# Kernel tuning notes

Measured on AMD Instinct MI355X. Metric: run time of the kernel, lower is better.

The kernel has to match this reference:

```python
import jax, jax.numpy as jnp
from jax import lax
import numpy as np

WSTD = 0.1
BSTD = 0.1
DN = ("NHWC", "HWIO", "NHWC")  # matches tf.nn.convolution defaults


def setup_inputs() -> dict:
    key = jax.random.key(0)
    k1, k2, k3, k4, k5 = jax.random.split(key, 5)
    B, H, Wd, Cin, F, KH, KW = 32, 64, 64, 128, 256, 3, 3
    X = jax.random.normal(k1, (B, H, Wd, Cin), dtype=jnp.float32)
    # glorot-ish kernel
    fan = KH * KW * Cin
    W = jax.random.normal(k2, (KH, KW, Cin, F), dtype=jnp.float32) / np.float32(np.sqrt(fan))
    bias = 0.01 * jax.random.normal(k3, (F,), dtype=jnp.float32)
    # per-sample multiplicative errors: abs(1 + N(0, std)) as in A-Connect
    Werr = jnp.abs(1.0 + WSTD * jax.random.normal(k4, (B, KH, KW, Cin, F), dtype=jnp.float32))
    Berr = jnp.abs(1.0 + BSTD * jax.random.normal(k5, (B, F), dtype=jnp.float32))
    return {"X": X, "W": W, "bias": bias, "Werr": Werr, "Berr": Berr}


def reference(X, W, bias, Werr, Berr):
    # memW[b] = W * Werr[b]  -> per-sample perturbed kernels [B,KH,KW,Cin,F]
    memW = W[None] * Werr

    def conv1(x, k):  # x: [H,W,Cin], k: [KH,KW,Cin,F]
        return lax.conv_general_dilated(x[None], k, window_strides=(1, 1),
                                        padding="SAME", dimension_numbers=DN)[0]

    Z = jax.vmap(conv1)(X, memW)                 # [B,H,W,F]
    membias = bias[None] * Berr                  # [B,F]
    Z = Z + membias[:, None, None, :]
    return jax.nn.relu(Z)
```

## Files before the change

### kernel.cpp

```cpp
#include <hip/hip_runtime.h>

#define B_   32
#define H_   64
#define W_   64
#define CIN  128
#define F_   256
#define K_   1152
#define M_   4096

#define HP_   66
#define XPROW (66*128)
#define XPIMG (66*66*128)
#define XP_ELEMS ((size_t)B_ * XPIMG)
#define XP_BYTES (XP_ELEMS * 2)

#define WBT_BYTES ((size_t)B_ * F_ * K_ * 2)
#define FULL_WS   (WBT_BYTES + XP_BYTES + 256)
#define ZPAGE_OFF WBT_BYTES

#define BM_ 256
#define BK_ 64

typedef __attribute__((ext_vector_type(8))) short bf16x8;
typedef __attribute__((ext_vector_type(4))) float f32x4;

__device__ __forceinline__ unsigned pkbf(float a, float b) {
    unsigned ua = __builtin_bit_cast(unsigned, a) + 0x8000u;
    unsigned ub = __builtin_bit_cast(unsigned, b) + 0x8000u;
    return __builtin_amdgcn_perm(ub, ua, 0x07060302u);
}

__device__ __forceinline__ void async16(const void* g, void* l) {
    __builtin_amdgcn_global_load_lds(
        (const __attribute__((address_space(1))) unsigned int*)g,
        (__attribute__((address_space(3))) unsigned int*)l, 16, 0, 0);
}

__global__ void prep_kernel(const float* __restrict__ W,
                            const float* __restrict__ Werr,
                            const float* __restrict__ X,
                            unsigned short* __restrict__ WbT,
                            unsigned short* __restrict__ Xp,
                            unsigned int* __restrict__ zpage) {
    __shared__ float tile[32 * 68];
    int bid = blockIdx.x;
    int t   = threadIdx.x;

    if (bid < 4608) {
        int ft   = bid & 3;
        int rest = bid >> 2;
        int kt   = rest % 36;
        int b    = rest / 36;
        int k0 = kt * 32;
        int f0 = ft * 64;

        if (bid == 0 && t < 64) zpage[t] = 0u;

        #pragma unroll
        for (int i = 0; i < 2; ++i) {
            int c   = i * 256 + t;
            int kl  = c >> 4;
            int fl4 = c & 15;
            size_t src = (size_t)(k0 + kl) * F_ + f0 + fl4 * 4;
            f32x4 w4 = *(const f32x4*)&W[src];
            f32x4 e4 = *(const f32x4*)&Werr[(size_t)b * (K_ * F_) + src];
            f32x4 v  = w4 * e4;
            *(f32x4*)&tile[kl * 68 + fl4 * 4] = v;
        }
        __syncthreads();
        {
            int c  = t;
            int fl = c >> 2;
            int ku = c & 3;
            unsigned pk[4];
            #pragma unroll
            for (int j2 = 0; j2 < 4; ++j2) {
                float x0 = tile[(ku * 8 + j2 * 2 + 0) * 68 + fl];
                float x1 = tile[(ku * 8 + j2 * 2 + 1) * 68 + fl];
                pk[j2] = pkbf(x0, x1);
            }
            size_t dst = ((size_t)(b * F_ + f0 + fl)) * K_ + k0 + ku * 8;
            *(uint4*)&WbT[dst] = make_uint4(pk[0], pk[1], pk[2], pk[3]);
        }
    } else {
        int e = (bid - 4608) * 256 + t;
        int c16  = e & 15;
        int pos  = e >> 4;
        int wp   = pos % 66;
        int rest = pos / 66;
        int hp   = rest % 66;
        int b    = rest / 66;
        uint4 out;
        if (hp >= 1 && hp <= 64 && wp >= 1 && wp <= 64) {
            const float* src = X + (((size_t)b * 64 + (hp - 1)) * 64 + (wp - 1)) * 128
                                 + c16 * 8;
            f32x4 a = *(const f32x4*)src;
            f32x4 c = *(const f32x4*)(src + 4);
            out.x = pkbf(a[0], a[1]);  out.y = pkbf(a[2], a[3]);
            out.z = pkbf(c[0], c[1]);  out.w = pkbf(c[2], c[3]);
        } else {
            out = make_uint4(0u, 0u, 0u, 0u);
        }
        *(uint4*)&Xp[(size_t)e * 8] = out;
    }
}

__global__ void wbt_kernel(const float* __restrict__ W,
                           const float* __restrict__ Werr,
                           unsigned short* __restrict__ WbT,
                           unsigned int* __restrict__ zpage) {
    __shared__ float tile[32 * 68];
    int bid = blockIdx.x;
    int ft   = bid & 3;
    int rest = bid >> 2;
    int kt   = rest % 36;
    int b    = rest / 36;
    int k0 = kt * 32;
    int f0 = ft * 64;
    int t  = threadIdx.x;

    if (bid == 0 && t < 64) zpage[t] = 0u;

    #pragma unroll
    for (int i = 0; i < 2; ++i) {
        int c   = i * 256 + t;
        int kl  = c >> 4;
        int fl4 = c & 15;
        size_t src = (size_t)(k0 + kl) * F_ + f0 + fl4 * 4;
        f32x4 w4 = *(const f32x4*)&W[src];
        f32x4 e4 = *(const f32x4*)&Werr[(size_t)b * (K_ * F_) + src];
        f32x4 v  = w4 * e4;
        *(f32x4*)&tile[kl * 68 + fl4 * 4] = v;
    }
    __syncthreads();
    {
        int c  = t;
        int fl = c >> 2;
        int ku = c & 3;
        unsigned pk[4];
        #pragma unroll
        for (int j2 = 0; j2 < 4; ++j2) {
            float x0 = tile[(ku * 8 + j2 * 2 + 0) * 68 + fl];
            float x1 = tile[(ku * 8 + j2 * 2 + 1) * 68 + fl];
            pk[j2] = pkbf(x0, x1);
        }
        size_t dst = ((size_t)(b * F_ + f0 + fl)) * K_ + k0 + ku * 8;
        *(uint4*)&WbT[dst] = make_uint4(pk[0], pk[1], pk[2], pk[3]);
    }
}

__global__ __launch_bounds__(512, 2)
void gemm256_kernel(const unsigned short* __restrict__ Xp,
                    const unsigned short* __restrict__ WbT,
                    const float* __restrict__ bias,
                    const float* __restrict__ Berr,
                    float* __restrict__ Out) {
    __shared__ unsigned short As[2][BM_ * BK_];
    __shared__ unsigned short Bs[2][BM_ * BK_];

    int bid = blockIdx.x;
    int g   = (bid & 7) * 64 + (bid >> 3);
    int b   = g >> 4;
    int mt  = g & 15;
    int pm0 = mt * 256;

    int t    = threadIdx.x;
    int lane = t & 63;
    int wv   = t >> 6;
    int wm   = wv >> 2;
    int wn   = wv & 3;
    int l16  = lane & 15;
    int quad = lane >> 4;
    int swz  = (l16 & 7) << 4;

    const unsigned short* XpB = Xp + (size_t)b * XPIMG;
    const unsigned short* WbB = WbT + (size_t)b * F_ * K_;

    int aofs[4], bofs[4], ldst[4];
    #pragma unroll
    for (int p = 0; p < 4; ++p) {
        int c   = p * 512 + t;
        int row = c >> 3;
        int col = c & 7;
        int sc  = col ^ (row & 7);
        int m   = pm0 + row;
        int hb  = m >> 6, ww = m & 63;
        aofs[p] = hb * XPROW + ww * 128 + sc * 8;
        bofs[p] = row * K_ + sc * 8;
        ldst[p] = c * 8;
    }

    f32x4 acc[8][4];
    #pragma unroll
    for (int mi = 0; mi < 8; ++mi)
        #pragma unroll
        for (int ni = 0; ni < 4; ++ni)
            acc[mi][ni] = (f32x4){0.f, 0.f, 0.f, 0.f};

    #pragma unroll
    for (int p = 0; p < 4; ++p)
        async16(XpB + aofs[p], &As[0][ldst[p]]);
    #pragma unroll
    for (int p = 0; p < 4; ++p)
        async16(WbB + bofs[p], &Bs[0][ldst[p]]);
    asm volatile("s_waitcnt vmcnt(0)" ::: "memory");
    __builtin_amdgcn_s_barrier();

    for (int kt = 0; kt < 18; ++kt) {
        const int cur = kt & 1;
        const unsigned short* Acur = As[cur];
        const unsigned short* Bcur = Bs[cur];
        unsigned short* Anxt = As[cur ^ 1];
        unsigned short* Bnxt = Bs[cur ^ 1];
        const bool pf = (kt < 17);

        int ktn  = kt + 1;
        int khwN = ktn >> 1;
        int khN  = (khwN * 11) >> 5;
        int kwN  = khwN - khN * 3;
        int koA  = khN * XPROW + kwN * 128 + (ktn & 1) * 64;
        int koB  = ktn * 64;

        bf16x8 bfr[4];
        #pragma unroll
        for (int ks = 0; ks < 2; ++ks) {
            #pragma unroll
            for (int qm = 0; qm < 2; ++qm) {
                if (qm == 0) {
                    #pragma unroll
                    for (int ni = 0; ni < 4; ++ni) {
                        int row = wn * 64 + ni * 16 + l16;
                        bfr[ni] = *(const bf16x8*)((const char*)Bcur +
                                   ((row * 128 + quad * 16 + ks * 64) ^ swz));
                    }
                }
                bf16x8 af[4];
                #pragma unroll
                for (int mi = 0; mi < 4; ++mi) {
                    int row = wm * 128 + (qm * 4 + mi) * 16 + l16;
                    af[mi] = *(const bf16x8*)((const char*)Acur +
                              ((row * 128 + quad * 16 + ks * 64) ^ swz));
                }

                if (pf && ks == 0) {
                    if (qm == 0) {
                        #pragma unroll
                        for (int p = 0; p < 4; ++p)
                            async16(XpB + aofs[p] + koA, &Anxt[ldst[p]]);
                    } else {
                        #pragma unroll
                        for (int p = 0; p < 4; ++p)
                            async16(WbB + bofs[p] + koB, &Bnxt[ldst[p]]);
                    }
                }

                __builtin_amdgcn_s_barrier();

                __builtin_amdgcn_s_setprio(1);
                #pragma unroll
                for (int mi = 0; mi < 4; ++mi)
                    #pragma unroll
                    for (int ni = 0; ni < 4; ++ni)
                        acc[qm * 4 + mi][ni] = __builtin_amdgcn_mfma_f32_16x16x32_bf16(
                            af[mi], bfr[ni], acc[qm * 4 + mi][ni], 0, 0, 0);
                __builtin_amdgcn_s_setprio(0);

                if (ks == 1 && qm == 1) {
                    if (pf) asm volatile("s_waitcnt vmcnt(0)" ::: "memory");
                    __builtin_amdgcn_s_barrier();
                } else {
                    __builtin_amdgcn_s_barrier();
                }
            }
        }
    }

    float mb[4];
    #pragma unroll
    for (int ni = 0; ni < 4; ++ni) {
        int f = wn * 64 + ni * 16 + l16;
        mb[ni] = bias[f] * Berr[b * F_ + f];
    }
    #pragma unroll
    for (int mi = 0; mi < 8; ++mi) {
        #pragma unroll
        for (int rr = 0; rr < 4; ++rr) {
            int mm = pm0 + wm * 128 + mi * 16 + quad * 4 + rr;
            float* orow = Out + ((size_t)b * M_ + mm) * F_ + wn * 64;
            #pragma unroll
            for (int ni = 0; ni < 4; ++ni) {
                float v = acc[mi][ni][rr] + mb[ni];
                orow[ni * 16 + l16] = fmaxf(v, 0.0f);
            }
        }
    }
}

__global__ __launch_bounds__(256, 2)
void gemm_kernel_f32(const float* __restrict__ X,
                     const unsigned short* __restrict__ WbT,
                     const float* __restrict__ zpage,
                     const float* __restrict__ bias,
                     const float* __restrict__ Berr,
                     float* __restrict__ Out) {
    __shared__ unsigned short As[128 * 32];
    __shared__ unsigned short Bs[128 * 32];

    int bid = blockIdx.x;
    int g   = (bid & 7) | ((bid >> 8) << 3);
    int mt  = (bid >> 3) & 31;
    int b   = g >> 1;
    int nt  = g & 1;
    int pm0 = mt * 128;

    int t    = threadIdx.x;
    int lane = t & 63;
    int wv   = t >> 6;
    int wm   = wv >> 1;
    int wn   = wv & 1;
    int l16  = lane & 15;
    int quad = lane >> 4;

    int ml   = t >> 1;
    int half = t & 1;
    int m    = pm0 + ml;
    int hb   = m >> 6;
    int wwv  = m & 63;
    const float* Abase = X + (((size_t)b * 64 + hb - 1) * 64 + (wwv - 1)) * 128
                           + half * 16;
    unsigned vm = 0;
    #pragma unroll
    for (int khw = 0; khw < 9; ++khw) {
        int kh = (khw * 11) >> 5;
        int kw = khw - kh * 3;
        bool ok = ((unsigned)(hb + kh - 1) < 64u) && ((unsigned)(wwv + kw - 1) < 64u);
        vm |= (unsigned)ok << khw;
    }
    int ldsA = ml * 32 + half * 16;

    const unsigned short* wb = WbT + ((size_t)(b * F_ + nt * 128)) * K_;
    const unsigned short* Bbase[2];
    int ldsB[2];
    #pragma unroll
    for (int cc = 0; cc < 2; ++cc) {
        int c   = t + cc * 256;
        int nl  = c >> 2;
        int off = c & 3;
        Bbase[cc] = wb + (size_t)nl * K_ + off * 8;
        ldsB[cc]  = c * 8;
    }

    f32x4 acc[4][4];
    #pragma unroll
    for (int mi = 0; mi < 4; ++mi)
        #pragma unroll
        for (int ni = 0; ni < 4; ++ni)
            acc[mi][ni] = (f32x4){0.f, 0.f, 0.f, 0.f};

    f32x4 pr0, pr1, pr2, pr3;
    {
        const float* p = (vm & 1) ? Abase : zpage;
        pr0 = *(const f32x4*)(p);
        pr1 = *(const f32x4*)(p + 4);
        pr2 = *(const f32x4*)(p + 8);
        pr3 = *(const f32x4*)(p + 12);
    }

    for (int kt = 0; kt < 36; ++kt) {
        uint4 lo, hi;
        lo.x = pkbf(pr0[0], pr0[1]);  lo.y = pkbf(pr0[2], pr0[3]);
        lo.z = pkbf(pr1[0], pr1[1]);  lo.w = pkbf(pr1[2], pr1[3]);
        hi.x = pkbf(pr2[0], pr2[1]);  hi.y = pkbf(pr2[2], pr2[3]);
        hi.z = pkbf(pr3[0], pr3[1]);  hi.w = pkbf(pr3[2], pr3[3]);

        if (kt) __syncthreads();
        *(uint4*)&As[ldsA]     = lo;
        *(uint4*)&As[ldsA + 8] = hi;
        #pragma unroll
        for (int cc = 0; cc < 2; ++cc)
            async16(Bbase[cc] + kt * 32, &Bs[ldsB[cc]]);
        __syncthreads();

        if (kt < 35) {
            int ktn  = kt + 1;
            int khw  = ktn >> 2;
            int kh   = (khw * 11) >> 5;
            int kw   = khw - kh * 3;
            int koff = kh * 8192 + kw * 128 + ((ktn & 3) << 5);
            const float* p = ((vm >> khw) & 1) ? Abase + koff : zpage;
            pr0 = *(const f32x4*)(p);
            pr1 = *(const f32x4*)(p + 4);
            pr2 = *(const f32x4*)(p + 8);
            pr3 = *(const f32x4*)(p + 12);
        }

        bf16x8 af[4], bf[4];
        #pragma unroll
        for (int i = 0; i < 4; ++i) {
            af[i] = *(const bf16x8*)&As[(wm * 64 + i * 16 + l16) * 32 + quad * 8];
            bf[i] = *(const bf16x8*)&Bs[(wn * 64 + i * 16 + l16) * 32 + quad * 8];
        }
        #pragma unroll
        for (int mi = 0; mi < 4; ++mi)
            #pragma unroll
            for (int ni = 0; ni < 4; ++ni)
                acc[mi][ni] = __builtin_amdgcn_mfma_f32_16x16x32_bf16(
                    af[mi], bf[ni], acc[mi][ni], 0, 0, 0);
    }

    float mb[4];
    #pragma unroll
    for (int ni = 0; ni < 4; ++ni) {
        int f = nt * 128 + wn * 64 + ni * 16 + l16;
        mb[ni] = bias[f] * Berr[b * F_ + f];
    }
    #pragma unroll
    for (int mi = 0; mi < 4; ++mi) {
        #pragma unroll
        for (int rr = 0; rr < 4; ++rr) {
            int mm = pm0 + wm * 64 + mi * 16 + quad * 4 + rr;
            float* orow = Out + ((size_t)b * M_ + mm) * F_ + nt * 128 + wn * 64;
            #pragma unroll
            for (int ni = 0; ni < 4; ++ni) {
                float v = acc[mi][ni][rr] + mb[ni];
                orow[ni * 16 + l16] = fmaxf(v, 0.0f);
            }
        }
    }
}

__global__ __launch_bounds__(256)
void fallback_kernel(const float* __restrict__ X, const float* __restrict__ W,
                     const float* __restrict__ bias, const float* __restrict__ Werr,
                     const float* __restrict__ Berr, float* __restrict__ Out) {
    __shared__ float Xs[3 * 66 * 128];
    int bid = blockIdx.x;
    int b = bid >> 6;
    int h = bid & 63;
    int t = threadIdx.x;
    int f = t;

    for (int e = t; e < 3 * 66 * 128; e += 256) {
        int kh  = e / (66 * 128);
        int rem = e - kh * 66 * 128;
        int w66 = rem >> 7;
        int c   = rem & 127;
        int hh = h + kh - 1, ww = w66 - 1;
        float v = 0.f;
        if (hh >= 0 && hh < 64 && ww >= 0 && ww < 64)
            v = X[(((size_t)b * 64 + hh) * 64 + ww) * 128 + c];
        Xs[e] = v;
    }
    __syncthreads();

    float acc[64];
    #pragma unroll
    for (int w = 0; w < 64; ++w) acc[w] = 0.f;

    for (int kk = 0; kk < 9; ++kk) {
        int kh = (kk * 11) >> 5;
        int kw = kk - kh * 3;
        for (int c = 0; c < 128; ++c) {
            size_t wi = ((size_t)kk * 128 + c) * 256 + f;
            float wvv = W[wi] * Werr[(size_t)b * (K_ * F_) + wi];
            const float* xr = &Xs[(kh * 66 + kw) * 128 + c];
            #pragma unroll
            for (int w = 0; w < 64; ++w)
                acc[w] = fmaf(xr[w * 128], wvv, acc[w]);
        }
    }
    float mb = bias[f] * Berr[b * 256 + f];
    for (int w = 0; w < 64; ++w)
        Out[(((size_t)b * 64 + h) * 64 + w) * 256 + f] = fmaxf(acc[w] + mb, 0.f);
}

extern "C" void kernel_launch(void* const* d_in, const int* in_sizes, int n_in,
                              void* d_out, int out_size, void* d_ws, size_t ws_size,
                              hipStream_t stream) {
    const float* X    = (const float*)d_in[0];
    const float* W    = (const float*)d_in[1];
    const float* bias = (const float*)d_in[2];
    const float* Werr = (const float*)d_in[3];
    const float* Berr = (const float*)d_in[4];
    float* Out = (float*)d_out;

    if (ws_size >= FULL_WS) {
        unsigned short* WbT = (unsigned short*)d_ws;
        unsigned short* Xp  = (unsigned short*)((char*)d_ws + WBT_BYTES);
        unsigned int*   zpg = (unsigned int*)((char*)d_ws + WBT_BYTES + XP_BYTES);
        prep_kernel<<<4608 + 8712, 256, 0, stream>>>(W, Werr, X, WbT, Xp, zpg);
        gemm256_kernel<<<512, 512, 0, stream>>>(Xp, WbT, bias, Berr, Out);
    } else if (ws_size >= WBT_BYTES + 256) {
        unsigned short* WbT  = (unsigned short*)d_ws;
        unsigned int*   zpg  = (unsigned int*)((char*)d_ws + ZPAGE_OFF);
        wbt_kernel<<<B_ * 36 * 4, 256, 0, stream>>>(W, Werr, WbT, zpg);
        gemm_kernel_f32<<<B_ * 32 * 2, 256, 0, stream>>>(X, WbT, (const float*)zpg,
                                                         bias, Berr, Out);
    } else {
        fallback_kernel<<<B_ * 64, 256, 0, stream>>>(X, W, bias, Werr, Berr, Out);
    }
}
```

Before: 311.2 us.

## Spread prefetch loads across phases and use partial vmcnt waits

Each k-tile's global-to-LDS prefetch is split into four two-load groups, one per compute phase. B is issued first and A last, so the wait before the next tile only needs `vmcnt(2)` rather than a full drain. Address math is simplified to one base offset plus per-row-unit strides, which frees the per-thread offset arrays and their registers. The risk is LDS ordering: the partial waits must be correct for the A rows read early in the next iteration, and the changed load order could add memory stalls.

After: 297.0 us. -4.6%, faster.

```diff
diff --git a/kernel.cpp b/kernel.cpp
--- a/kernel.cpp
+++ b/kernel.cpp
@@ -176,19 +176,12 @@
     const unsigned short* XpB = Xp + (size_t)b * XPIMG;
     const unsigned short* WbB = WbT + (size_t)b * F_ * K_;
 
-    int aofs[4], bofs[4], ldst[4];
-    #pragma unroll
-    for (int p = 0; p < 4; ++p) {
-        int c   = p * 512 + t;
-        int row = c >> 3;
-        int col = c & 7;
-        int sc  = col ^ (row & 7);
-        int m   = pm0 + row;
-        int hb  = m >> 6, ww = m & 63;
-        aofs[p] = hb * XPROW + ww * 128 + sc * 8;
-        bofs[p] = row * K_ + sc * 8;
-        ldst[p] = c * 8;
-    }
+    int tr   = t >> 3;
+    int sc   = (t & 7) ^ (tr & 7);
+    int aoff = tr * 128 + sc * 8;
+    int boff = tr * K_ + sc * 8;
+    int mbase = mt * 4;
+    int ldof = t * 8;
 
     f32x4 acc[8][4];
     #pragma unroll
@@ -197,21 +190,25 @@
         for (int ni = 0; ni < 4; ++ni)
             acc[mi][ni] = (f32x4){0.f, 0.f, 0.f, 0.f};
 
-    #pragma unroll
-    for (int p = 0; p < 4; ++p)
-        async16(XpB + aofs[p], &As[0][ldst[p]]);
-    #pragma unroll
-    for (int p = 0; p < 4; ++p)
-        async16(WbB + bofs[p], &Bs[0][ldst[p]]);
-    asm volatile("s_waitcnt vmcnt(0)" ::: "memory");
+    auto stageA = [&](int bs, int ru, int ko) {
+        async16(XpB + (size_t)(mbase + ru) * XPROW + aoff + ko,
+                &As[bs][ru * 4096 + ldof]);
+    };
+    auto stageB = [&](int bs, int ru, int ko) {
+        async16(WbB + (size_t)ru * (64 * K_) + boff + ko,
+                &Bs[bs][ru * 4096 + ldof]);
+    };
+
+    stageB(0, 0, 0); stageB(0, 1, 0); stageB(0, 2, 0); stageB(0, 3, 0);
+    stageA(0, 0, 0); stageA(0, 2, 0); stageA(0, 1, 0); stageA(0, 3, 0);
+    asm volatile("s_waitcnt vmcnt(2)" ::: "memory");
     __builtin_amdgcn_s_barrier();
 
     for (int kt = 0; kt < 18; ++kt) {
         const int cur = kt & 1;
-        const unsigned short* Acur = As[cur];
-        const unsigned short* Bcur = Bs[cur];
-        unsigned short* Anxt = As[cur ^ 1];
-        unsigned short* Bnxt = Bs[cur ^ 1];
+        const int nxt = cur ^ 1;
+        const unsigned short* Ac = As[cur];
+        const unsigned short* Bc = Bs[cur];
         const bool pf = (kt < 17);
 
         int ktn  = kt + 1;
@@ -221,58 +218,88 @@
         int koA  = khN * XPROW + kwN * 128 + (ktn & 1) * 64;
         int koB  = ktn * 64;
 
-        bf16x8 bfr[4];
-        #pragma unroll
-        for (int ks = 0; ks < 2; ++ks) {
-            #pragma unroll
-            for (int qm = 0; qm < 2; ++qm) {
-                if (qm == 0) {
-                    #pragma unroll
-                    for (int ni = 0; ni < 4; ++ni) {
-                        int row = wn * 64 + ni * 16 + l16;
-                        bfr[ni] = *(const bf16x8*)((const char*)Bcur +
-                                   ((row * 128 + quad * 16 + ks * 64) ^ swz));
-                    }
-                }
-                bf16x8 af[4];
-                #pragma unroll
-                for (int mi = 0; mi < 4; ++mi) {
-                    int row = wm * 128 + (qm * 4 + mi) * 16 + l16;
-                    af[mi] = *(const bf16x8*)((const char*)Acur +
-                              ((row * 128 + quad * 16 + ks * 64) ^ swz));
-                }
-
-                if (pf && ks == 0) {
-                    if (qm == 0) {
-                        #pragma unroll
-                        for (int p = 0; p < 4; ++p)
-                            async16(XpB + aofs[p] + koA, &Anxt[ldst[p]]);
-                    } else {
-                        #pragma unroll
-                        for (int p = 0; p < 4; ++p)
-                            async16(WbB + bofs[p] + koB, &Bnxt[ldst[p]]);
-                    }
-                }
-
-                __builtin_amdgcn_s_barrier();
-
-                __builtin_amdgcn_s_setprio(1);
-                #pragma unroll
-                for (int mi = 0; mi < 4; ++mi)
-                    #pragma unroll
-                    for (int ni = 0; ni < 4; ++ni)
-                        acc[qm * 4 + mi][ni] = __builtin_amdgcn_mfma_f32_16x16x32_bf16(
-                            af[mi], bfr[ni], acc[qm * 4 + mi][ni], 0, 0, 0);
-                __builtin_amdgcn_s_setprio(0);
-
-                if (ks == 1 && qm == 1) {
-                    if (pf) asm volatile("s_waitcnt vmcnt(0)" ::: "memory");
-                    __builtin_amdgcn_s_barrier();
-                } else {
-                    __builtin_amdgcn_s_barrier();
-                }
-            }
-        }
+        bf16x8 af[4], bfr[4];
+
+        #pragma unroll
+        for (int ni = 0; ni < 4; ++ni) {
+            int row = wn * 64 + ni * 16 + l16;
+            bfr[ni] = *(const bf16x8*)((const char*)Bc + ((row * 128 + quad * 16) ^ swz));
+        }
+        #pragma unroll
+        for (int mi = 0; mi < 4; ++mi) {
+            int row = wm * 128 + mi * 16 + l16;
+            af[mi] = *(const bf16x8*)((const char*)Ac + ((row * 128 + quad * 16) ^ swz));
+        }
+        if (pf) { stageB(nxt, 0, koB); stageB(nxt, 1, koB); }
+        __builtin_amdgcn_s_barrier();
+        __builtin_amdgcn_s_setprio(1);
+        #pragma unroll
+        for (int mi = 0; mi < 4; ++mi)
+            #pragma unroll
+            for (int ni = 0; ni < 4; ++ni)
+                acc[mi][ni] = __builtin_amdgcn_mfma_f32_16x16x32_bf16(
+                    af[mi], bfr[ni], acc[mi][ni], 0, 0, 0);
+        __builtin_amdgcn_s_setprio(0);
+        if (pf) asm volatile("s_waitcnt vmcnt(2)" ::: "memory");
+        else    asm volatile("s_waitcnt vmcnt(0)" ::: "memory");
+        __builtin_amdgcn_s_barrier();
+
+        #pragma unroll
+        for (int mi = 0; mi < 4; ++mi) {
+            int row = wm * 128 + 64 + mi * 16 + l16;
+            af[mi] = *(const bf16x8*)((const char*)Ac + ((row * 128 + quad * 16) ^ swz));
+        }
+        if (pf) { stageB(nxt, 2, koB); stageB(nxt, 3, koB); }
+        __builtin_amdgcn_s_barrier();
+        __builtin_amdgcn_s_setprio(1);
+        #pragma unroll
+        for (int mi = 0; mi < 4; ++mi)
+            #pragma unroll
+            for (int ni = 0; ni < 4; ++ni)
+                acc[4 + mi][ni] = __builtin_amdgcn_mfma_f32_16x16x32_bf16(
+                    af[mi], bfr[ni], acc[4 + mi][ni], 0, 0, 0);
+        __builtin_amdgcn_s_setprio(0);
+        __builtin_amdgcn_s_barrier();
+
+        #pragma unroll
+        for (int ni = 0; ni < 4; ++ni) {
+            int row = wn * 64 + ni * 16 + l16;
+            bfr[ni] = *(const bf16x8*)((const char*)Bc + ((row * 128 + quad * 16 + 64) ^ swz));
+        }
+        #pragma unroll
+        for (int mi = 0; mi < 4; ++mi) {
+            int row = wm * 128 + mi * 16 + l16;
+            af[mi] = *(const bf16x8*)((const char*)Ac + ((row * 128 + quad * 16 + 64) ^ swz));
+        }
+        if (pf) { stageA(nxt, 0, koA); stageA(nxt, 2, koA); }
+        __builtin_amdgcn_s_barrier();
+        __builtin_amdgcn_s_setprio(1);
+        #pragma unroll
+        for (int mi = 0; mi < 4; ++mi)
+            #pragma unroll
+            for (int ni = 0; ni < 4; ++ni)
+                acc[mi][ni] = __builtin_amdgcn_mfma_f32_16x16x32_bf16(
+                    af[mi], bfr[ni], acc[mi][ni], 0, 0, 0);
+        __builtin_amdgcn_s_setprio(0);
+        __builtin_amdgcn_s_barrier();
+
+        #pragma unroll
+        for (int mi = 0; mi < 4; ++mi) {
+            int row = wm * 128 + 64 + mi * 16 + l16;
+            af[mi] = *(const bf16x8*)((const char*)Ac + ((row * 128 + quad * 16 + 64) ^ swz));
+        }
+        if (pf) { stageA(nxt, 1, koA); stageA(nxt, 3, koA); }
+        __builtin_amdgcn_s_barrier();
+        __builtin_amdgcn_s_setprio(1);
+        #pragma unroll
+        for (int mi = 0; mi < 4; ++mi)
+            #pragma unroll
+            for (int ni = 0; ni < 4; ++ni)
+                acc[4 + mi][ni] = __builtin_amdgcn_mfma_f32_16x16x32_bf16(
+                    af[mi], bfr[ni], acc[4 + mi][ni], 0, 0, 0);
+        __builtin_amdgcn_s_setprio(0);
+        if (pf) asm volatile("s_waitcnt vmcnt(2)" ::: "memory");
+        __builtin_amdgcn_s_barrier();
     }
 
     float mb[4];
```

## Restructure GEMM main loop into fine-grained half-tile async load pipeline

Applied to the files above, without the earlier changes.

Replaces the double-buffered K loop with a manually unrolled two-tile-per-iteration schedule. Global-to-LDS loads for the next tile are issued in half-tile chunks interleaved between MFMA phases, with partial vmcnt waits and scheduler barriers. The aim is to keep more loads in flight and overlap memory latency with compute more evenly. The cost is more barriers and a complex wait-count scheme that could easily be wrong or over-serialize.

After: 301.1 us. -3.2%, faster.

```diff
diff --git a/kernel.cpp b/kernel.cpp
--- a/kernel.cpp
+++ b/kernel.cpp
@@ -35,6 +35,9 @@
         (const __attribute__((address_space(1))) unsigned int*)g,
         (__attribute__((address_space(3))) unsigned int*)l, 16, 0, 0);
 }
+
+#define PHB do { __builtin_amdgcn_s_barrier(); \
+                 __builtin_amdgcn_sched_barrier(0); } while (0)
 
 __global__ void prep_kernel(const float* __restrict__ W,
                             const float* __restrict__ Werr,
@@ -176,18 +179,19 @@
     const unsigned short* XpB = Xp + (size_t)b * XPIMG;
     const unsigned short* WbB = WbT + (size_t)b * F_ * K_;
 
-    int aofs[4], bofs[4], ldst[4];
-    #pragma unroll
-    for (int p = 0; p < 4; ++p) {
-        int c   = p * 512 + t;
-        int row = c >> 3;
+    int asrc[2][2], bsrc[2][2];
+    #pragma unroll
+    for (int cc = 0; cc < 2; ++cc) {
+        int c   = t + cc * 512;
+        int r16 = c >> 3;
         int col = c & 7;
-        int sc  = col ^ (row & 7);
-        int m   = pm0 + row;
-        int hb  = m >> 6, ww = m & 63;
-        aofs[p] = hb * XPROW + ww * 128 + sc * 8;
-        bofs[p] = row * K_ + sc * 8;
-        ldst[p] = c * 8;
+        #pragma unroll
+        for (int h = 0; h < 2; ++h) {
+            int row = h * 128 + r16;
+            int sc  = col ^ (row & 7);
+            asrc[h][cc] = (mt * 4 + (row >> 6)) * XPROW + (row & 63) * 128 + sc * 8;
+            bsrc[h][cc] = row * K_ + sc * 8;
+        }
     }
 
     f32x4 acc[8][4];
@@ -197,82 +201,109 @@
         for (int ni = 0; ni < 4; ++ni)
             acc[mi][ni] = (f32x4){0.f, 0.f, 0.f, 0.f};
 
-    #pragma unroll
-    for (int p = 0; p < 4; ++p)
-        async16(XpB + aofs[p], &As[0][ldst[p]]);
-    #pragma unroll
-    for (int p = 0; p < 4; ++p)
-        async16(WbB + bofs[p], &Bs[0][ldst[p]]);
-    asm volatile("s_waitcnt vmcnt(0)" ::: "memory");
-    __builtin_amdgcn_s_barrier();
-
-    for (int kt = 0; kt < 18; ++kt) {
-        const int cur = kt & 1;
-        const unsigned short* Acur = As[cur];
-        const unsigned short* Bcur = Bs[cur];
-        unsigned short* Anxt = As[cur ^ 1];
-        unsigned short* Bnxt = Bs[cur ^ 1];
-        const bool pf = (kt < 17);
-
-        int ktn  = kt + 1;
-        int khwN = ktn >> 1;
-        int khN  = (khwN * 11) >> 5;
-        int kwN  = khwN - khN * 3;
-        int koA  = khN * XPROW + kwN * 128 + (ktn & 1) * 64;
-        int koB  = ktn * 64;
-
-        bf16x8 bfr[4];
-        #pragma unroll
-        for (int ks = 0; ks < 2; ++ks) {
+    auto stA = [&](int buf, int h, int ko) {
+        async16(XpB + asrc[h][0] + ko, &As[buf][h * 8192 + t * 8]);
+        async16(XpB + asrc[h][1] + ko, &As[buf][h * 8192 + 4096 + t * 8]);
+    };
+    auto stB = [&](int buf, int h, int ko) {
+        async16(WbB + bsrc[h][0] + ko, &Bs[buf][h * 8192 + t * 8]);
+        async16(WbB + bsrc[h][1] + ko, &Bs[buf][h * 8192 + 4096 + t * 8]);
+    };
+    auto rdB = [&](bf16x8* dst, const unsigned short* Bc, int ks) {
+        #pragma unroll
+        for (int ni = 0; ni < 4; ++ni) {
+            int row = wn * 64 + ni * 16 + l16;
+            dst[ni] = *(const bf16x8*)((const char*)Bc +
+                       ((row * 128 + quad * 16 + ks * 64) ^ swz));
+        }
+    };
+    auto rdA = [&](bf16x8* dst, const unsigned short* Ac, int qm, int ks) {
+        #pragma unroll
+        for (int mi = 0; mi < 4; ++mi) {
+            int row = wm * 128 + qm * 64 + mi * 16 + l16;
+            dst[mi] = *(const bf16x8*)((const char*)Ac +
+                       ((row * 128 + quad * 16 + ks * 64) ^ swz));
+        }
+    };
+    auto mm = [&](int qm, const bf16x8* a, const bf16x8* bb) {
+        __builtin_amdgcn_s_setprio(1);
+        #pragma unroll
+        for (int mi = 0; mi < 4; ++mi)
             #pragma unroll
-            for (int qm = 0; qm < 2; ++qm) {
-                if (qm == 0) {
-                    #pragma unroll
-                    for (int ni = 0; ni < 4; ++ni) {
-                        int row = wn * 64 + ni * 16 + l16;
-                        bfr[ni] = *(const bf16x8*)((const char*)Bcur +
-                                   ((row * 128 + quad * 16 + ks * 64) ^ swz));
-                    }
-                }
-                bf16x8 af[4];
-                #pragma unroll
-                for (int mi = 0; mi < 4; ++mi) {
-                    int row = wm * 128 + (qm * 4 + mi) * 16 + l16;
-                    af[mi] = *(const bf16x8*)((const char*)Acur +
-                              ((row * 128 + quad * 16 + ks * 64) ^ swz));
-                }
-
-                if (pf && ks == 0) {
-                    if (qm == 0) {
-                        #pragma unroll
-                        for (int p = 0; p < 4; ++p)
-                            async16(XpB + aofs[p] + koA, &Anxt[ldst[p]]);
-                    } else {
-                        #pragma unroll
-                        for (int p = 0; p < 4; ++p)
-                            async16(WbB + bofs[p] + koB, &Bnxt[ldst[p]]);
-                    }
-                }
-
-                __builtin_amdgcn_s_barrier();
-
-                __builtin_amdgcn_s_setprio(1);
-                #pragma unroll
-                for (int mi = 0; mi < 4; ++mi)
-                    #pragma unroll
-                    for (int ni = 0; ni < 4; ++ni)
-                        acc[qm * 4 + mi][ni] = __builtin_amdgcn_mfma_f32_16x16x32_bf16(
-                            af[mi], bfr[ni], acc[qm * 4 + mi][ni], 0, 0, 0);
-                __builtin_amdgcn_s_setprio(0);
-
-                if (ks == 1 && qm == 1) {
-                    if (pf) asm volatile("s_waitcnt vmcnt(0)" ::: "memory");
-                    __builtin_amdgcn_s_barrier();
-                } else {
-                    __builtin_amdgcn_s_barrier();
-                }
-            }
-        }
+            for (int ni = 0; ni < 4; ++ni)
+                acc[qm * 4 + mi][ni] = __builtin_amdgcn_mfma_f32_16x16x32_bf16(
+                    a[mi], bb[ni], acc[qm * 4 + mi][ni], 0, 0, 0);
+        __builtin_amdgcn_s_setprio(0);
+    };
+
+    stB(0, 0, 0); stB(0, 1, 0); stA(0, 0, 0); stA(0, 1, 0); stB(1, 0, 64);
+    asm volatile("s_waitcnt vmcnt(4)" ::: "memory");
+    PHB;
+
+    for (int p = 0; p < 9; ++p) {
+        const bool pf = (p < 8);
+        int kh_o = (p * 11) >> 5;
+        int kw_o = p - 3 * kh_o;
+        int koA_o = kh_o * XPROW + kw_o * 128 + 64;
+        int koB_o = (2 * p + 1) * 64;
+        int q1 = p + 1;
+        int kh_e = (q1 * 11) >> 5;
+        int kw_e = q1 - 3 * kh_e;
+        int koA_e2 = kh_e * XPROW + kw_e * 128;
+        int koB_e2 = (2 * p + 2) * 64;
+        int koB_o2 = (2 * p + 3) * 64;
+
+        const unsigned short* A0 = As[0]; const unsigned short* B0 = Bs[0];
+        const unsigned short* A1 = As[1]; const unsigned short* B1 = Bs[1];
+
+        bf16x8 bb[4], aa[4];
+
+        rdB(bb, B0, 0); rdA(aa, A0, 0, 0);
+        stB(1, 1, koB_o);
+        PHB;
+        mm(0, aa, bb);
+        asm volatile("s_waitcnt vmcnt(4)" ::: "memory");
+        PHB;
+        rdA(aa, A0, 1, 0);
+        stA(1, 0, koA_o);
+        PHB;
+        mm(1, aa, bb);
+        PHB;
+        rdB(bb, B0, 1); rdA(aa, A0, 0, 1);
+        stA(1, 1, koA_o);
+        PHB;
+        mm(0, aa, bb);
+        PHB;
+        rdA(aa, A0, 1, 1);
+        if (pf) stB(0, 0, koB_e2);
+        PHB;
+        mm(1, aa, bb);
+        if (pf) asm volatile("s_waitcnt vmcnt(4)" ::: "memory");
+        else    asm volatile("s_waitcnt vmcnt(2)" ::: "memory");
+        PHB;
+        rdB(bb, B1, 0); rdA(aa, A1, 0, 0);
+        if (pf) stB(0, 1, koB_e2);
+        PHB;
+        mm(0, aa, bb);
+        if (pf) asm volatile("s_waitcnt vmcnt(4)" ::: "memory");
+        else    asm volatile("s_waitcnt vmcnt(0)" ::: "memory");
+        PHB;
+        rdA(aa, A1, 1, 0);
+        if (pf) stA(0, 0, koA_e2);
+        PHB;
+        mm(1, aa, bb);
+        PHB;
+        rdB(bb, B1, 1); rdA(aa, A1, 0, 1);
+        if (pf) stA(0, 1, koA_e2);
+        PHB;
+        mm(0, aa, bb);
+        PHB;
+        rdA(aa, A1, 1, 1);
+        if (pf) stB(1, 0, koB_o2);
+        PHB;
+        mm(1, aa, bb);
+        if (pf) asm volatile("s_waitcnt vmcnt(4)" ::: "memory");
+        PHB;
     }
 
     float mb[4];
@@ -285,8 +316,8 @@
     for (int mi = 0; mi < 8; ++mi) {
         #pragma unroll
         for (int rr = 0; rr < 4; ++rr) {
-            int mm = pm0 + wm * 128 + mi * 16 + quad * 4 + rr;
-            float* orow = Out + ((size_t)b * M_ + mm) * F_ + wn * 64;
+            int mm2 = pm0 + wm * 128 + mi * 16 + quad * 4 + rr;
+            float* orow = Out + ((size_t)b * M_ + mm2) * F_ + wn * 64;
             #pragma unroll
             for (int ni = 0; ni < 4; ++ni) {
                 float v = acc[mi][ni][rr] + mb[ni];
```

## Switch conv GEMM to 128x256 tiles with triple-buffered BK=32 async pipeline

Applied to the files above, without the earlier changes.

The main bf16 GEMM moves from a 256x256 tile with BK=64 and double buffering to a 128x256 tile with BK=32 and a three-stage LDS ring. The launch doubles to 1024 blocks and the launch bound rises to 4 waves per SIMD. Prefetches now stay two stages ahead using partial vmcnt waits, with sched_barrier to stop the compiler reordering across phases. The goal is more occupancy and better latency hiding, at the cost of more B-tile reloads per output and less register reuse per block.

Measured after the change: 297.1 us. 1.05x faster.

```diff
diff --git a/kernel.cpp b/kernel.cpp
--- a/kernel.cpp
+++ b/kernel.cpp
@@ -18,9 +18,6 @@
 #define FULL_WS   (WBT_BYTES + XP_BYTES + 256)
 #define ZPAGE_OFF WBT_BYTES
 
-#define BM_ 256
-#define BK_ 64
-
 typedef __attribute__((ext_vector_type(8))) short bf16x8;
 typedef __attribute__((ext_vector_type(4))) float f32x4;
 
@@ -35,6 +32,9 @@
         (const __attribute__((address_space(1))) unsigned int*)g,
         (__attribute__((address_space(3))) unsigned int*)l, 16, 0, 0);
 }
+
+#define PHB do { __builtin_amdgcn_s_barrier(); \
+                 __builtin_amdgcn_sched_barrier(0); } while (0)
 
 __global__ void prep_kernel(const float* __restrict__ W,
                             const float* __restrict__ Werr,
@@ -149,20 +149,20 @@
     }
 }
 
-__global__ __launch_bounds__(512, 2)
-void gemm256_kernel(const unsigned short* __restrict__ Xp,
+__global__ __launch_bounds__(512, 4)
+void gemm128_kernel(const unsigned short* __restrict__ Xp,
                     const unsigned short* __restrict__ WbT,
                     const float* __restrict__ bias,
                     const float* __restrict__ Berr,
                     float* __restrict__ Out) {
-    __shared__ unsigned short As[2][BM_ * BK_];
-    __shared__ unsigned short Bs[2][BM_ * BK_];
+    __shared__ unsigned short As[3][128 * 32];
+    __shared__ unsigned short Bs[3][256 * 32];
 
     int bid = blockIdx.x;
-    int g   = (bid & 7) * 64 + (bid >> 3);
-    int b   = g >> 4;
-    int mt  = g & 15;
-    int pm0 = mt * 256;
+    int g   = (bid & 7) * 128 + (bid >> 3);
+    int b   = g >> 5;
+    int mt  = g & 31;
+    int pm0 = mt * 128;
 
     int t    = threadIdx.x;
     int lane = t & 63;
@@ -171,109 +171,82 @@
     int wn   = wv & 3;
     int l16  = lane & 15;
     int quad = lane >> 4;
-    int swz  = (l16 & 7) << 4;
+    int rswz = ((l16 >> 1) & 3) << 4;
 
     const unsigned short* XpB = Xp + (size_t)b * XPIMG;
     const unsigned short* WbB = WbT + (size_t)b * F_ * K_;
 
-    int aofs[4], bofs[4], ldst[4];
-    #pragma unroll
-    for (int p = 0; p < 4; ++p) {
-        int c   = p * 512 + t;
-        int row = c >> 3;
-        int col = c & 7;
-        int sc  = col ^ (row & 7);
-        int m   = pm0 + row;
-        int hb  = m >> 6, ww = m & 63;
-        aofs[p] = hb * XPROW + ww * 128 + sc * 8;
-        bofs[p] = row * K_ + sc * 8;
-        ldst[p] = c * 8;
-    }
-
-    f32x4 acc[8][4];
-    #pragma unroll
-    for (int mi = 0; mi < 8; ++mi)
+    int sc    = (t & 3) ^ ((t >> 3) & 3);
+    int arow  = t >> 2;
+    int aoff  = (mt * 2 + (arow >> 6)) * XPROW + (arow & 63) * 128 + sc * 8;
+    int boff0 = (t >> 2) * K_ + sc * 8;
+    int boff1 = (128 + (t >> 2)) * K_ + sc * 8;
+
+    f32x4 acc[4][4];
+    #pragma unroll
+    for (int mi = 0; mi < 4; ++mi)
         #pragma unroll
         for (int ni = 0; ni < 4; ++ni)
             acc[mi][ni] = (f32x4){0.f, 0.f, 0.f, 0.f};
 
-    #pragma unroll
-    for (int p = 0; p < 4; ++p)
-        async16(XpB + aofs[p], &As[0][ldst[p]]);
-    #pragma unroll
-    for (int p = 0; p < 4; ++p)
-        async16(WbB + bofs[p], &Bs[0][ldst[p]]);
-    asm volatile("s_waitcnt vmcnt(0)" ::: "memory");
-    __builtin_amdgcn_s_barrier();
-
-    for (int kt = 0; kt < 18; ++kt) {
-        const int cur = kt & 1;
-        const unsigned short* Acur = As[cur];
-        const unsigned short* Bcur = Bs[cur];
-        unsigned short* Anxt = As[cur ^ 1];
-        unsigned short* Bnxt = Bs[cur ^ 1];
-        const bool pf = (kt < 17);
-
-        int ktn  = kt + 1;
-        int khwN = ktn >> 1;
-        int khN  = (khwN * 11) >> 5;
-        int kwN  = khwN - khN * 3;
-        int koA  = khN * XPROW + kwN * 128 + (ktn & 1) * 64;
-        int koB  = ktn * 64;
-
-        bf16x8 bfr[4];
-        #pragma unroll
-        for (int ks = 0; ks < 2; ++ks) {
-            #pragma unroll
-            for (int qm = 0; qm < 2; ++qm) {
-                if (qm == 0) {
-                    #pragma unroll
-                    for (int ni = 0; ni < 4; ++ni) {
-                        int row = wn * 64 + ni * 16 + l16;
-                        bfr[ni] = *(const bf16x8*)((const char*)Bcur +
-                                   ((row * 128 + quad * 16 + ks * 64) ^ swz));
-                    }
-                }
-                bf16x8 af[4];
-                #pragma unroll
-                for (int mi = 0; mi < 4; ++mi) {
-                    int row = wm * 128 + (qm * 4 + mi) * 16 + l16;
-                    af[mi] = *(const bf16x8*)((const char*)Acur +
-                              ((row * 128 + quad * 16 + ks * 64) ^ swz));
-                }
-
-                if (pf && ks == 0) {
-                    if (qm == 0) {
-                        #pragma unroll
-                        for (int p = 0; p < 4; ++p)
-                            async16(XpB + aofs[p] + koA, &Anxt[ldst[p]]);
-                    } else {
-                        #pragma unroll
-                        for (int p = 0; p < 4; ++p)
-                            async16(WbB + bofs[p] + koB, &Bnxt[ldst[p]]);
-                    }
-                }
-
-                __builtin_amdgcn_s_barrier();
-
-                __builtin_amdgcn_s_setprio(1);
-                #pragma unroll
-                for (int mi = 0; mi < 4; ++mi)
-                    #pragma unroll
-                    for (int ni = 0; ni < 4; ++ni)
-                        acc[qm * 4 + mi][ni] = __builtin_amdgcn_mfma_f32_16x16x32_bf16(
-                            af[mi], bfr[ni], acc[qm * 4 + mi][ni], 0, 0, 0);
-                __builtin_amdgcn_s_setprio(0);
-
-                if (ks == 1 && qm == 1) {
-                    if (pf) asm volatile("s_waitcnt vmcnt(0)" ::: "memory");
-                    __builtin_amdgcn_s_barrier();
-                } else {
-                    __builtin_amdgcn_s_barrier();
-                }
-            }
-        }
-    }
+    auto koffA = [&](int kt) {
+        int khw = kt >> 2;
+        int kh  = (khw * 11) >> 5;
+        int kw  = khw - 3 * kh;
+        return kh * XPROW + kw * 128 + (kt & 3) * 32;
+    };
+
+    auto stage = [&](int buf, int kt) {
+        int ka = koffA(kt);
+        int kb = kt * 32;
+        async16(XpB + aoff + ka,  &As[buf][t * 8]);
+        async16(WbB + boff0 + kb, &Bs[buf][t * 8]);
+        async16(WbB + boff1 + kb, &Bs[buf][(t + 512) * 8]);
+    };
+
+    auto iter = [&](const unsigned short* Ac, const unsigned short* Bc,
+                    int stbuf, int stkt, int gate) {
+        bf16x8 af[4], bf[4];
+        #pragma unroll
+        for (int mi = 0; mi < 4; ++mi) {
+            int row = wm * 64 + mi * 16 + l16;
+            af[mi] = *(const bf16x8*)((const char*)Ac +
+                      ((row * 64 + quad * 16) ^ rswz));
+        }
+        #pragma unroll
+        for (int ni = 0; ni < 4; ++ni) {
+            int row = wn * 64 + ni * 16 + l16;
+            bf[ni] = *(const bf16x8*)((const char*)Bc +
+                      ((row * 64 + quad * 16) ^ rswz));
+        }
+        if (stbuf >= 0) stage(stbuf, stkt);
+        __builtin_amdgcn_s_setprio(1);
+        #pragma unroll
+        for (int mi = 0; mi < 4; ++mi)
+            #pragma unroll
+            for (int ni = 0; ni < 4; ++ni)
+                acc[mi][ni] = __builtin_amdgcn_mfma_f32_16x16x32_bf16(
+                    af[mi], bf[ni], acc[mi][ni], 0, 0, 0);
+        __builtin_amdgcn_s_setprio(0);
+        if (gate == 3)      asm volatile("s_waitcnt vmcnt(3)" ::: "memory");
+        else if (gate == 0) asm volatile("s_waitcnt vmcnt(0)" ::: "memory");
+        if (gate >= 0) PHB;
+    };
+
+    stage(0, 0);
+    stage(1, 1);
+    asm volatile("s_waitcnt vmcnt(3)" ::: "memory");
+    PHB;
+
+    for (int k3 = 0; k3 < 11; ++k3) {
+        int kt = k3 * 3;
+        iter(As[0], Bs[0], 2, kt + 2, 3);
+        iter(As[1], Bs[1], 0, kt + 3, 3);
+        iter(As[2], Bs[2], 1, kt + 4, 3);
+    }
+    iter(As[0], Bs[0], 2, 35, 3);
+    iter(As[1], Bs[1], -1, 0, 0);
+    iter(As[2], Bs[2], -1, 0, -1);
 
     float mb[4];
     #pragma unroll
@@ -282,10 +255,10 @@
         mb[ni] = bias[f] * Berr[b * F_ + f];
     }
     #pragma unroll
-    for (int mi = 0; mi < 8; ++mi) {
+    for (int mi = 0; mi < 4; ++mi) {
         #pragma unroll
         for (int rr = 0; rr < 4; ++rr) {
-            int mm = pm0 + wm * 128 + mi * 16 + quad * 4 + rr;
+            int mm = pm0 + wm * 64 + mi * 16 + quad * 4 + rr;
             float* orow = Out + ((size_t)b * M_ + mm) * F_ + wn * 64;
             #pragma unroll
             for (int ni = 0; ni < 4; ++ni) {
@@ -489,7 +462,7 @@
         unsigned short* Xp  = (unsigned short*)((char*)d_ws + WBT_BYTES);
         unsigned int*   zpg = (unsigned int*)((char*)d_ws + WBT_BYTES + XP_BYTES);
         prep_kernel<<<4608 + 8712, 256, 0, stream>>>(W, Werr, X, WbT, Xp, zpg);
-        gemm256_kernel<<<512, 512, 0, stream>>>(Xp, WbT, bias, Berr, Out);
+        gemm128_kernel<<<1024, 512, 0, stream>>>(Xp, WbT, bias, Berr, Out);
     } else if (ws_size >= WBT_BYTES + 256) {
         unsigned short* WbT  = (unsigned short*)d_ws;
         unsigned int*   zpg  = (unsigned int*)((char*)d_ws + ZPAGE_OFF);
```
